# Kernel optimization log

Measured on AMD Instinct MI355X. Metric: run time of the kernel, lower is better.

The kernel has to match this reference:

```python
import jax, jax.numpy as jnp
import numpy as np

N_ENT, N_REL, RANK, B = 40000, 1200, 200, 500
INIT = 1e-3


def _lorentz_rotate(lhs, rot):
    # lhs: [B, d, 5], rot: [B, d, 4]; quaternion rotation of spatial part
    rot = jax.nn.gelu(rot, approximate=False)  # torch F.gelu default = exact erf
    t, r, i, j, k = (lhs[..., m:m + 1] for m in range(5))
    rr, ri, rj, rk = (rot[..., m:m + 1] for m in range(4))
    A = r * rr - i * ri - j * rj - k * rk
    Bq = r * ri + rr * i + j * rk - rj * k
    C = r * rj + rr * j + k * ri - rk * i
    D = r * rk + rr * k + i * rj - ri * j
    return jnp.concatenate([t, A, Bq, C, D], axis=-1)


def _lorentz_boost2(lhs, boost):
    # lhs: [B, d, 5], boost: [B, d, 4]
    b = jax.nn.sigmoid(boost) / 4.0
    t, s = lhs[..., 0:1], lhs[..., 1:]               # [B,d,1], [B,d,4]
    b2 = jnp.sum(b * b, axis=-1, keepdims=True)      # [B,d,1]
    eye = jnp.eye(4, dtype=lhs.dtype)
    bb = jnp.sqrt(eye + b[..., :, None] * b[..., None, :])  # [B,d,4,4]
    xt = t * b2 + jnp.sum(b * s, axis=-1, keepdims=True)
    xs = t * b + jnp.einsum('bdij,bdj->bdi', bb, s)
    return jnp.concatenate([xt, xs], axis=-1)


def setup_inputs() -> dict:
    key = jax.random.key(0)
    k1, k2, k3, k4 = jax.random.split(key, 4)
    ent = jax.random.normal(k1, (N_ENT, RANK, 5), jnp.float32) * INIT
    ent = ent / jnp.linalg.norm(ent, axis=-1, keepdims=True)  # param_init normalization
    rot = jax.random.normal(k2, (N_REL, RANK, 4), jnp.float32) * INIT
    boo = jax.random.normal(k3, (N_REL, RANK, 4), jnp.float32) * INIT
    queries = jax.random.randint(k4, (B, 3), 0, 1000, jnp.int32)
    return {'queries': queries, 'ent_embedding': ent, 'rel_rotate': rot, 'rel_boosts': boo}


def reference(queries, ent_embedding, rel_rotate, rel_boosts):
    lhs = ent_embedding[queries[:, 0]]     # [B, d, 5]
    rot = rel_rotate[queries[:, 1]]        # [B, d, 4]
    boost = rel_boosts[queries[:, 1]]      # [B, d, 4]
    lhs = _lorentz_rotate(lhs, rot)
    lhs = _lorentz_boost2(lhs, boost)
    # cinner: negate time component of x, contract over (d,5), mean over d
    x = lhs.at[..., 0].multiply(-1.0)
    d = ent_embedding.shape[1]
    cin = jnp.einsum('bdi,ndi->bn', x, ent_embedding) / d  # [B, n_ent]
    scores = 2.0 + 2.0 * cin  # -( -2 - 2*cinner )
    reg_rel = jnp.sqrt(jnp.sum(rot ** 2, axis=-1)) + jnp.sqrt(jnp.sum(boost ** 2, axis=-1))
    return scores, reg_rel
```

## Files before the change

kernel.cpp:

```cpp
#include <hip/hip_runtime.h>
#include <hip/hip_bf16.h>
#include <math.h>

#define N_ENT   40000
#define RANK    200
#define NB      500
#define K_REAL  1000
#define K_PAD   1024
#define M_PAD   512

typedef __attribute__((ext_vector_type(8))) short       short8;
typedef __attribute__((ext_vector_type(4))) float       f32x4;
typedef __attribute__((ext_vector_type(4))) unsigned short ushort4v;
typedef __attribute__((ext_vector_type(8))) unsigned short ushort8v;

__device__ __forceinline__ unsigned short f2bf(float f) {
    union { float f; unsigned int u; } v; v.f = f;
    unsigned int u = v.u;
    return (unsigned short)((u + 0x7FFFu + ((u >> 16) & 1u)) >> 16);
}

__device__ __forceinline__ void gld_lds16(const void* g, void* l) {
    __builtin_amdgcn_global_load_lds(
        (const __attribute__((address_space(1))) unsigned int*)g,
        (__attribute__((address_space(3))) unsigned int*)l,
        16, 0, 0);
}

__global__ __launch_bounds__(256) void lkg_cvt(
    const float4* __restrict__ in, ushort4v* __restrict__ outv, int n4)
{
    int i = blockIdx.x * 256 + threadIdx.x;
    const int stride = gridDim.x * 256;
    for (; i < n4; i += stride) {
        const float4 v = in[i];
        ushort4v w;
        w.x = f2bf(v.x); w.y = f2bf(v.y); w.z = f2bf(v.z); w.w = f2bf(v.w);
        outv[i] = w;
    }
}

__global__ __launch_bounds__(256) void lkg_prep(
    const int* __restrict__ queries,
    const float* __restrict__ ent,
    const float* __restrict__ rot,
    const float* __restrict__ boo,
    unsigned short* __restrict__ xws,
    float* __restrict__ out)
{
    const int b   = blockIdx.x;
    const int tid = threadIdx.x;
    unsigned short* xrow = xws + (size_t)b * K_PAD;

    if (b >= NB) {
        ((uint2*)xrow)[tid] = make_uint2(0u, 0u);
        return;
    }
    if (tid >= RANK) {
        int c = tid - RANK;
        if (c < K_PAD - K_REAL) xrow[K_REAL + c] = 0;
        return;
    }

    const int d  = tid;
    const int q0 = queries[b * 3 + 0];
    const int q1 = queries[b * 3 + 1];

    const float* L  = ent + (size_t)q0 * (RANK * 5) + d * 5;
    const float* R  = rot + (size_t)q1 * (RANK * 4) + d * 4;
    const float* Bo = boo + (size_t)q1 * (RANK * 4) + d * 4;

    const float t = L[0], r = L[1], i = L[2], j = L[3], k = L[4];
    const float r0 = R[0],  r1 = R[1],  r2 = R[2],  r3 = R[3];
    const float o0 = Bo[0], o1 = Bo[1], o2 = Bo[2], o3 = Bo[3];

    out[(size_t)NB * N_ENT + (size_t)b * RANK + d] =
        sqrtf(r0*r0 + r1*r1 + r2*r2 + r3*r3) +
        sqrtf(o0*o0 + o1*o1 + o2*o2 + o3*o3);

    const float is2 = 0.70710678118654752440f;
    const float rr = 0.5f * r0 * (1.0f + erff(r0 * is2));
    const float ri = 0.5f * r1 * (1.0f + erff(r1 * is2));
    const float rj = 0.5f * r2 * (1.0f + erff(r2 * is2));
    const float rk = 0.5f * r3 * (1.0f + erff(r3 * is2));

    const float s0 = r*rr - i*ri - j*rj - k*rk;
    const float s1 = r*ri + rr*i + j*rk - rj*k;
    const float s2 = r*rj + rr*j + k*ri - rk*i;
    const float s3 = r*rk + rr*k + i*rj - ri*j;

    const float b0 = 0.25f / (1.0f + expf(-o0));
    const float b1 = 0.25f / (1.0f + expf(-o1));
    const float b2 = 0.25f / (1.0f + expf(-o2));
    const float b3 = 0.25f / (1.0f + expf(-o3));

    const float bsq = b0*b0 + b1*b1 + b2*b2 + b3*b3;
    const float xt  = t * bsq + b0*s0 + b1*s1 + b2*s2 + b3*s3;

    const float m00 = sqrtf(1.0f + b0*b0), m11 = sqrtf(1.0f + b1*b1);
    const float m22 = sqrtf(1.0f + b2*b2), m33 = sqrtf(1.0f + b3*b3);
    const float m01 = sqrtf(b0*b1), m02 = sqrtf(b0*b2), m03 = sqrtf(b0*b3);
    const float m12 = sqrtf(b1*b2), m13 = sqrtf(b1*b3), m23 = sqrtf(b2*b3);

    const float xs0 = t*b0 + m00*s0 + m01*s1 + m02*s2 + m03*s3;
    const float xs1 = t*b1 + m01*s0 + m11*s1 + m12*s2 + m13*s3;
    const float xs2 = t*b2 + m02*s0 + m12*s1 + m22*s2 + m23*s3;
    const float xs3 = t*b3 + m03*s0 + m13*s1 + m23*s2 + m33*s3;

    unsigned short* w = xrow + d * 5;
    w[0] = f2bf(-xt);
    w[1] = f2bf(xs0);
    w[2] = f2bf(xs1);
    w[3] = f2bf(xs2);
    w[4] = f2bf(xs3);
}

__global__ __launch_bounds__(256) void lkg_gemm2(
    const unsigned short* __restrict__ xbf,
    const unsigned short* __restrict__ ebf,
    float* __restrict__ out)
{
    __shared__ unsigned short As[128 * 32];
    __shared__ unsigned short Bs[128 * 32];

    const int bm  = blockIdx.x;
    const int n0  = blockIdx.y * 128;
    const int tid = threadIdx.x;
    const int wave = tid >> 6, lane = tid & 63;
    const int wy = wave >> 1, wx = wave & 1;
    const int l15 = lane & 15, quad = lane >> 4;

    f32x4 acc[4][4] = {};

    for (int kt = 0; kt < 32; ++kt) {
        #pragma unroll
        for (int ii = 0; ii < 2; ++ii) {
            const int c = tid + ii * 256;
            gld_lds16(xbf + (size_t)(bm * 128 + (c >> 2)) * K_PAD + kt * 32 + (c & 3) * 8,
                      (void*)(As + c * 8));
        }
        if (kt < 31) {
            #pragma unroll
            for (int ii = 0; ii < 2; ++ii) {
                const int c = tid + ii * 256;
                gld_lds16(ebf + (size_t)(n0 + (c >> 2)) * K_REAL + kt * 32 + (c & 3) * 8,
                          (void*)(Bs + c * 8));
            }
        } else if (tid < 128) {
            const ushort8v v = *(const ushort8v*)(ebf + (size_t)(n0 + tid) * K_REAL + 992);
            *(ushort8v*)(Bs + tid * 32) = v;
        }
        __syncthreads();

        short8 a[4], bf[4];
        #pragma unroll
        for (int mi = 0; mi < 4; ++mi)
            a[mi] = *(const short8*)(As + (wy * 64 + mi * 16 + l15) * 32 + quad * 8);
        #pragma unroll
        for (int ni = 0; ni < 4; ++ni)
            bf[ni] = *(const short8*)(Bs + (wx * 64 + ni * 16 + l15) * 32 + quad * 8);

        #pragma unroll
        for (int mi = 0; mi < 4; ++mi)
            #pragma unroll
            for (int ni = 0; ni < 4; ++ni)
                acc[mi][ni] = __builtin_amdgcn_mfma_f32_16x16x32_bf16(
                    a[mi], bf[ni], acc[mi][ni], 0, 0, 0);
        __syncthreads();
    }

    #pragma unroll
    for (int mi = 0; mi < 4; ++mi) {
        const int gmb = bm * 128 + wy * 64 + mi * 16 + quad * 4;
        #pragma unroll
        for (int ni = 0; ni < 4; ++ni) {
            const int gn = n0 + wx * 64 + ni * 16 + l15;
            #pragma unroll
            for (int rr2 = 0; rr2 < 4; ++rr2) {
                const int gm = gmb + rr2;
                if (gm < NB && gn < N_ENT)
                    out[(size_t)gm * N_ENT + gn] = 2.0f + acc[mi][ni][rr2] * 0.01f;
            }
        }
    }
}

__global__ __launch_bounds__(256) void lkg_gemm(
    const unsigned short* __restrict__ xws,
    const float* __restrict__ ent,
    float* __restrict__ out)
{
    __shared__ unsigned short As[128 * 32];
    __shared__ unsigned short Bs[128 * 32];

    const int bm  = blockIdx.x;
    const int n0  = blockIdx.y * 128;
    const int tid = threadIdx.x;
    const int wave = tid >> 6, lane = tid & 63;
    const int wy = wave >> 1, wx = wave & 1;
    const int l15 = lane & 15, quad = lane >> 4;

    f32x4 acc[4][4] = {};

    for (int kt = 0; kt < K_PAD / 32; ++kt) {
        #pragma unroll
        for (int ii = 0; ii < 2; ++ii) {
            const int c   = tid + ii * 256;
            const int row = c >> 2, col = c & 3;
            const ushort8v v = *(const ushort8v*)(
                xws + (size_t)(bm * 128 + row) * K_PAD + kt * 32 + col * 8);
            *(ushort8v*)(As + row * 32 + col * 8) = v;
        }
        #pragma unroll
        for (int ii = 0; ii < 4; ++ii) {
            const int c   = tid + ii * 256;
            const int row = c >> 3, cc = c & 7;
            const int n = n0 + row;
            const int k = kt * 32 + cc * 4;
            float4 v = make_float4(0.f, 0.f, 0.f, 0.f);
            if (n < N_ENT && k < K_REAL)
                v = *(const float4*)(ent + (size_t)n * K_REAL + k);
            ushort4v w;
            w.x = f2bf(v.x); w.y = f2bf(v.y); w.z = f2bf(v.z); w.w = f2bf(v.w);
            *(ushort4v*)(Bs + row * 32 + cc * 4) = w;
        }
        __syncthreads();

        short8 a[4], bf[4];
        #pragma unroll
        for (int mi = 0; mi < 4; ++mi)
            a[mi] = *(const short8*)(As + (wy * 64 + mi * 16 + l15) * 32 + quad * 8);
        #pragma unroll
        for (int ni = 0; ni < 4; ++ni)
            bf[ni] = *(const short8*)(Bs + (wx * 64 + ni * 16 + l15) * 32 + quad * 8);

        #pragma unroll
        for (int mi = 0; mi < 4; ++mi)
            #pragma unroll
            for (int ni = 0; ni < 4; ++ni)
                acc[mi][ni] = __builtin_amdgcn_mfma_f32_16x16x32_bf16(
                    a[mi], bf[ni], acc[mi][ni], 0, 0, 0);
        __syncthreads();
    }

    #pragma unroll
    for (int mi = 0; mi < 4; ++mi) {
        const int gmb = bm * 128 + wy * 64 + mi * 16 + quad * 4;
        #pragma unroll
        for (int ni = 0; ni < 4; ++ni) {
            const int gn = n0 + wx * 64 + ni * 16 + l15;
            #pragma unroll
            for (int rr2 = 0; rr2 < 4; ++rr2) {
                const int gm = gmb + rr2;
                if (gm < NB && gn < N_ENT)
                    out[(size_t)gm * N_ENT + gn] = 2.0f + acc[mi][ni][rr2] * 0.01f;
            }
        }
    }
}

extern "C" void kernel_launch(void* const* d_in, const int* in_sizes, int n_in,
                              void* d_out, int out_size, void* d_ws, size_t ws_size,
                              hipStream_t stream) {
    const int*   queries = (const int*)d_in[0];
    const float* ent     = (const float*)d_in[1];
    const float* rot     = (const float*)d_in[2];
    const float* boo     = (const float*)d_in[3];
    float*       out     = (float*)d_out;

    const size_t NEED = (size_t)N_ENT * K_REAL * 2 + (size_t)M_PAD * K_PAD * 2;

    if (ws_size >= NEED) {
        unsigned short* ebf = (unsigned short*)d_ws;
        unsigned short* xbf = ebf + (size_t)N_ENT * K_REAL;
        lkg_cvt<<<4096, 256, 0, stream>>>((const float4*)ent, (ushort4v*)ebf,
                                          N_ENT * K_REAL / 4);
        lkg_prep<<<M_PAD, 256, 0, stream>>>(queries, ent, rot, boo, xbf, out);
        lkg_gemm2<<<dim3(4, (N_ENT + 127) / 128), 256, 0, stream>>>(xbf, ebf, out);
    } else {
        unsigned short* xws = (unsigned short*)d_ws;
        lkg_prep<<<M_PAD, 256, 0, stream>>>(queries, ent, rot, boo, xws, out);
        lkg_gemm<<<dim3(4, (N_ENT + 127) / 128), 256, 0, stream>>>(xws, ent, out);
    }
}
```

Baseline: 339.8 us.

## Double-buffer GEMM LDS tiles, stage epilogue through LDS, widen bf16 conversion stores

The bf16 GEMM now uses two LDS buffers so the loads for the next K tile are issued while MFMAs run on the current one, with one barrier per iteration. The epilogue stages accumulators through padded LDS so each thread writes the score matrix with coalesced float4 stores instead of scattered scalar stores. The fp32-to-bf16 conversion kernel now handles 8 elements per thread with 16-byte stores. The cost is doubled LDS use (which may lower occupancy) and extra barriers in the epilogue.

```diff
diff --git a/kernel.cpp b/kernel.cpp
--- a/kernel.cpp
+++ b/kernel.cpp
@@ -28,14 +28,15 @@
 }
 
 __global__ __launch_bounds__(256) void lkg_cvt(
-    const float4* __restrict__ in, ushort4v* __restrict__ outv, int n4)
+    const float4* __restrict__ in, ushort8v* __restrict__ outv, int n8)
 {
     int i = blockIdx.x * 256 + threadIdx.x;
     const int stride = gridDim.x * 256;
-    for (; i < n4; i += stride) {
-        const float4 v = in[i];
-        ushort4v w;
-        w.x = f2bf(v.x); w.y = f2bf(v.y); w.z = f2bf(v.z); w.w = f2bf(v.w);
+    for (; i < n8; i += stride) {
+        const float4 a = in[2 * i], b = in[2 * i + 1];
+        ushort8v w;
+        w[0] = f2bf(a.x); w[1] = f2bf(a.y); w[2] = f2bf(a.z); w[3] = f2bf(a.w);
+        w[4] = f2bf(b.x); w[5] = f2bf(b.y); w[6] = f2bf(b.z); w[7] = f2bf(b.w);
         outv[i] = w;
     }
 }
@@ -115,13 +116,12 @@
     w[4] = f2bf(xs3);
 }
 
-__global__ __launch_bounds__(256) void lkg_gemm2(
+__global__ __launch_bounds__(256) void lkg_gemm3(
     const unsigned short* __restrict__ xbf,
     const unsigned short* __restrict__ ebf,
     float* __restrict__ out)
 {
-    __shared__ unsigned short As[128 * 32];
-    __shared__ unsigned short Bs[128 * 32];
+    __shared__ __align__(16) unsigned short sm[16384];
 
     const int bm  = blockIdx.x;
     const int n0  = blockIdx.y * 128;
@@ -132,33 +132,52 @@
 
     f32x4 acc[4][4] = {};
 
+    #define STAGE_A(kt, buf)                                                      \
+        do {                                                                      \
+            _Pragma("unroll")                                                     \
+            for (int ii = 0; ii < 2; ++ii) {                                      \
+                const int c = tid + ii * 256;                                     \
+                gld_lds16(xbf + (size_t)(bm * 128 + (c >> 2)) * K_PAD             \
+                              + (kt) * 32 + (c & 3) * 8,                          \
+                          (void*)(sm + (buf) * 4096 + c * 8));                    \
+            }                                                                     \
+        } while (0)
+
+    #define STAGE_B(kt, buf)                                                      \
+        do {                                                                      \
+            if ((kt) < 31) {                                                      \
+                _Pragma("unroll")                                                 \
+                for (int ii = 0; ii < 2; ++ii) {                                  \
+                    const int c = tid + ii * 256;                                 \
+                    gld_lds16(ebf + (size_t)(n0 + (c >> 2)) * K_REAL              \
+                                  + (kt) * 32 + (c & 3) * 8,                      \
+                              (void*)(sm + 8192 + (buf) * 4096 + c * 8));         \
+                }                                                                 \
+            } else if (tid < 128) {                                               \
+                const ushort8v v = *(const ushort8v*)(                            \
+                    ebf + (size_t)(n0 + tid) * K_REAL + 992);                     \
+                *(ushort8v*)(sm + 8192 + (buf) * 4096 + tid * 32) = v;            \
+            }                                                                     \
+        } while (0)
+
+    STAGE_A(0, 0);
+    STAGE_B(0, 0);
+    __syncthreads();
+
     for (int kt = 0; kt < 32; ++kt) {
-        #pragma unroll
-        for (int ii = 0; ii < 2; ++ii) {
-            const int c = tid + ii * 256;
-            gld_lds16(xbf + (size_t)(bm * 128 + (c >> 2)) * K_PAD + kt * 32 + (c & 3) * 8,
-                      (void*)(As + c * 8));
-        }
-        if (kt < 31) {
-            #pragma unroll
-            for (int ii = 0; ii < 2; ++ii) {
-                const int c = tid + ii * 256;
-                gld_lds16(ebf + (size_t)(n0 + (c >> 2)) * K_REAL + kt * 32 + (c & 3) * 8,
-                          (void*)(Bs + c * 8));
-            }
-        } else if (tid < 128) {
-            const ushort8v v = *(const ushort8v*)(ebf + (size_t)(n0 + tid) * K_REAL + 992);
-            *(ushort8v*)(Bs + tid * 32) = v;
-        }
-        __syncthreads();
+        const int cur = kt & 1;
+        if (kt < 31) { STAGE_A(kt + 1, cur ^ 1); STAGE_B(kt + 1, cur ^ 1); }
+
+        const unsigned short* Ab = sm + cur * 4096;
+        const unsigned short* Bb = sm + 8192 + cur * 4096;
 
         short8 a[4], bf[4];
         #pragma unroll
         for (int mi = 0; mi < 4; ++mi)
-            a[mi] = *(const short8*)(As + (wy * 64 + mi * 16 + l15) * 32 + quad * 8);
+            a[mi] = *(const short8*)(Ab + (wy * 64 + mi * 16 + l15) * 32 + quad * 8);
         #pragma unroll
         for (int ni = 0; ni < 4; ++ni)
-            bf[ni] = *(const short8*)(Bs + (wx * 64 + ni * 16 + l15) * 32 + quad * 8);
+            bf[ni] = *(const short8*)(Bb + (wx * 64 + ni * 16 + l15) * 32 + quad * 8);
 
         #pragma unroll
         for (int mi = 0; mi < 4; ++mi)
@@ -166,20 +185,36 @@
             for (int ni = 0; ni < 4; ++ni)
                 acc[mi][ni] = __builtin_amdgcn_mfma_f32_16x16x32_bf16(
                     a[mi], bf[ni], acc[mi][ni], 0, 0, 0);
+
         __syncthreads();
     }
-
+    #undef STAGE_A
+    #undef STAGE_B
+
+    const int EPLD = 132;
+    float* ep = (float*)sm;
     #pragma unroll
     for (int mi = 0; mi < 4; ++mi) {
-        const int gmb = bm * 128 + wy * 64 + mi * 16 + quad * 4;
-        #pragma unroll
-        for (int ni = 0; ni < 4; ++ni) {
-            const int gn = n0 + wx * 64 + ni * 16 + l15;
+        if (mi) __syncthreads();
+        #pragma unroll
+        for (int ni = 0; ni < 4; ++ni)
             #pragma unroll
-            for (int rr2 = 0; rr2 < 4; ++rr2) {
-                const int gm = gmb + rr2;
-                if (gm < NB && gn < N_ENT)
-                    out[(size_t)gm * N_ENT + gn] = 2.0f + acc[mi][ni][rr2] * 0.01f;
+            for (int r = 0; r < 4; ++r)
+                ep[(wy * 16 + quad * 4 + r) * EPLD + wx * 64 + ni * 16 + l15] =
+                    acc[mi][ni][r];
+        __syncthreads();
+        #pragma unroll
+        for (int p = 0; p < 4; ++p) {
+            const int lrow = (tid >> 5) + p * 8;
+            const int col  = (tid & 31) * 4;
+            const int wyy = lrow >> 4, within = lrow & 15;
+            const int grow = bm * 128 + wyy * 64 + mi * 16 + within;
+            if (grow < NB && n0 + col < N_ENT) {
+                const float4 v = *(const float4*)(ep + lrow * EPLD + col);
+                float4 o;
+                o.x = 2.0f + 0.01f * v.x; o.y = 2.0f + 0.01f * v.y;
+                o.z = 2.0f + 0.01f * v.z; o.w = 2.0f + 0.01f * v.w;
+                *(float4*)(out + (size_t)grow * N_ENT + n0 + col) = o;
             }
         }
     }
@@ -273,10 +308,10 @@
     if (ws_size >= NEED) {
         unsigned short* ebf = (unsigned short*)d_ws;
         unsigned short* xbf = ebf + (size_t)N_ENT * K_REAL;
-        lkg_cvt<<<4096, 256, 0, stream>>>((const float4*)ent, (ushort4v*)ebf,
-                                          N_ENT * K_REAL / 4);
+        lkg_cvt<<<4096, 256, 0, stream>>>((const float4*)ent, (ushort8v*)ebf,
+                                          N_ENT * K_REAL / 8);
         lkg_prep<<<M_PAD, 256, 0, stream>>>(queries, ent, rot, boo, xbf, out);
-        lkg_gemm2<<<dim3(4, (N_ENT + 127) / 128), 256, 0, stream>>>(xbf, ebf, out);
+        lkg_gemm3<<<dim3(4, (N_ENT + 127) / 128), 256, 0, stream>>>(xbf, ebf, out);
     } else {
         unsigned short* xws = (unsigned short*)d_ws;
         lkg_prep<<<M_PAD, 256, 0, stream>>>(queries, ent, rot, boo, xws, out);
```

After: 342.5 us. No clear change (+0.8%).
